# Kernel tuning notes

Measured on AMD Instinct MI355X. Metric: run time of the kernel, lower is better.

Reference implementation:

```python
import jax, jax.numpy as jnp
import numpy as np

ALPHA = 0.2  # LeakyReLU negative slope
OUT_FEATURES = 128


def setup_inputs() -> dict:
    key = jax.random.key(0)
    k1, k2, k3 = jax.random.split(key, 3)
    B, N, F_in, F_out = 4, 4096, 128, OUT_FEATURES
    h = jax.random.normal(k1, (B, N, F_in), dtype=jnp.float32)
    # xavier_uniform with gain 1.414: bound = gain * sqrt(6/(fan_in+fan_out))
    bw = 1.414 * np.sqrt(6.0 / (F_in + F_out))
    W = jax.random.uniform(k2, (F_in, F_out), minval=-bw, maxval=bw, dtype=jnp.float32)
    ba = 1.414 * np.sqrt(6.0 / (2 * F_out + 1))
    a = jax.random.uniform(k3, (2 * F_out, 1), minval=-ba, maxval=ba, dtype=jnp.float32)
    return {"h": h, "W": W, "a": a}


def reference(h, W, a):
    # Wh: [B, N, F_out]
    Wh = jnp.einsum("bni,ij->bnj", h, W)
    a1 = a[:OUT_FEATURES, :]   # [F_out, 1]
    a2 = a[OUT_FEATURES:, :]   # [F_out, 1]
    Wh1 = jnp.einsum("bni,ij->bnj", Wh, a1)  # [B, N, 1]
    Wh2 = jnp.einsum("bni,ij->bnj", Wh, a2)  # [B, N, 1]
    # e: [B, N, N] via broadcast add of column + row vectors
    e = Wh1 + jnp.swapaxes(Wh2, 1, 2)
    e = jax.nn.leaky_relu(e, negative_slope=ALPHA)
    attention = jax.nn.softmax(e, axis=2)
    # dropout is identity in eval mode (p=0.0 / training=False)
    h_prime = jnp.einsum("bij,bjn->bin", attention, Wh)
    return jax.nn.elu(h_prime)
```

## Files before the change

kernel.cpp:

```cpp
#include <hip/hip_runtime.h>
#include <hip/hip_bf16.h>


#define ALPHA 0.2f
#define NN 4096
#define FD 128

typedef __attribute__((ext_vector_type(8))) short s8v;
typedef __attribute__((ext_vector_type(4))) float f4v;
typedef __attribute__((ext_vector_type(2))) unsigned int u2v;
typedef __attribute__((ext_vector_type(4))) unsigned int u4v;

__device__ __forceinline__ unsigned short f2bf(float x) {
  return (unsigned short)((__float_as_uint(x) + 0x8000u) >> 16);
}
__device__ __forceinline__ float bf2f(unsigned short s) {
  return __uint_as_float(((unsigned)s) << 16);
}

__global__ __launch_bounds__(256, 4) void k1_gemm(
    const float* __restrict__ h, const float* __restrict__ W,
    const float* __restrict__ a,
    unsigned short* __restrict__ WhTt,
    float* __restrict__ s1g, float* __restrict__ Eg, float* __restrict__ Fg)
{
  __shared__ __align__(16) unsigned char wls[32768];
  const int tid = threadIdx.x;
  const int b = blockIdx.x >> 6;
  const int j0 = (blockIdx.x & 63) << 6;

#pragma unroll
  for (int it = 0; it < 16; ++it) {
    int cidx = it * 256 + tid;
    int i = cidx >> 5;
    int f0 = (cidx & 31) << 2;
    f4v v = *(const f4v*)(W + (size_t)cidx * 4);
#pragma unroll
    for (int e = 0; e < 4; ++e) {
      int f = f0 + e;
      int byte = f * 256 + (((i >> 3) ^ (f & 15)) << 4) + ((i & 7) << 1);
      *(unsigned short*)(wls + byte) = f2bf(v[e]);
    }
  }
  __syncthreads();

  const int w = tid >> 6, lane = tid & 63;
  const int quad = lane >> 4, lcol = lane & 15;
  const int jrow = j0 + 16 * w + lcol;

  f4v acc[8];
#pragma unroll
  for (int nt = 0; nt < 8; ++nt) acc[nt] = (f4v){0.f, 0.f, 0.f, 0.f};

#pragma unroll
  for (int kk = 0; kk < 4; ++kk) {
    const float* hp = h + (((size_t)(b * NN + jrow)) << 7) + (kk << 5) + (quad << 3);
    f4v v0 = *(const f4v*)hp;
    f4v v1 = *(const f4v*)(hp + 4);
    s8v af;
#pragma unroll
    for (int e = 0; e < 4; ++e) { af[e] = (short)f2bf(v0[e]); af[4+e] = (short)f2bf(v1[e]); }
#pragma unroll
    for (int nt = 0; nt < 8; ++nt) {
      int f = 16 * nt + lcol;
      int slot = ((kk << 2) + quad) ^ (f & 15);
      s8v bfr = *(const s8v*)(wls + (f << 8) + (slot << 4));
      acc[nt] = __builtin_amdgcn_mfma_f32_16x16x32_bf16(af, bfr, acc[nt], 0, 0, 0);
    }
  }

  float s1v[4] = {0,0,0,0}, s2v[4] = {0,0,0,0};
#pragma unroll
  for (int nt = 0; nt < 8; ++nt) {
    float a1 = a[16 * nt + lcol];
    float a2 = a[128 + 16 * nt + lcol];
#pragma unroll
    for (int r = 0; r < 4; ++r) { s1v[r] += acc[nt][r] * a1; s2v[r] += acc[nt][r] * a2; }
  }
#pragma unroll
  for (int r = 0; r < 4; ++r)
#pragma unroll
    for (int d = 1; d < 16; d <<= 1) {
      s1v[r] += __shfl_xor(s1v[r], d, 64);
      s2v[r] += __shfl_xor(s2v[r], d, 64);
    }
  if (lcol == 0) {
    int jb = b * NN + j0 + 16 * w + (quad << 2);
    *(f4v*)(s1g + jb) = (f4v){s1v[0], s1v[1], s1v[2], s1v[3]};
    f4v Ee, Ff;
#pragma unroll
    for (int r = 0; r < 4; ++r) {
      float d = s2v[r] - 8.0f;
      Ee[r] = __expf(d);
      Ff[r] = __expf(ALPHA * d);
    }
    *(f4v*)(Eg + jb) = Ee;
    *(f4v*)(Fg + jb) = Ff;
  }

  {
    const int c = j0 >> 8;
    const int octb = ((j0 & 255) >> 3) + 2 * w + (quad >> 1);
    const int eoff = (quad & 1) << 2;
#pragma unroll
    for (int nt = 0; nt < 8; ++nt) {
      int f = 16 * nt + lcol;
      unsigned u0 = __float_as_uint(acc[nt][0]) + 0x8000u;
      unsigned u1 = __float_as_uint(acc[nt][1]) + 0x8000u;
      unsigned u2 = __float_as_uint(acc[nt][2]) + 0x8000u;
      unsigned u3 = __float_as_uint(acc[nt][3]) + 0x8000u;
      u2v pk;
      pk[0] = (u0 >> 16) | (u1 & 0xFFFF0000u);
      pk[1] = (u2 >> 16) | (u3 & 0xFFFF0000u);
      size_t off = ((((size_t)(b * 16 + c) * 32 + octb) * 128 + f) << 3) + eoff;
      *(u2v*)(WhTt + off) = pk;
    }
  }
}

__global__ __launch_bounds__(256, 2) void k3_split(
    const unsigned short* __restrict__ WhTt,
    const float* __restrict__ s1g,
    const float* __restrict__ Eg,
    const float* __restrict__ Fg,
    unsigned short* __restrict__ pO,
    float* __restrict__ pl)
{
  __shared__ __align__(16) unsigned char smem[24576];
  const int tid = threadIdx.x;
  const int w = tid >> 6, lane = tid & 63;
  const int quad = lane >> 4, lcol = lane & 15;
  const int blk = blockIdx.x;
  const int b = blk >> 7, rg = (blk >> 2) & 31, jq = blk & 3;
  const int irow0 = rg * 128 + w * 32;

  const unsigned short* whtb = WhTt + ((size_t)b << 19);
  const float* Egb = Eg + b * NN + (jq << 10);
  const float* Fgb = Fg + b * NN + (jq << 10);

  float rr[2];
#pragma unroll
  for (int mt = 0; mt < 2; ++mt) {
    float x = s1g[b * NN + irow0 + 16 * mt + lcol] + 8.0f;
    rr[mt] = __expf((ALPHA - 1.0f) * x);
  }

  {
    f4v ve = *(const f4v*)(Egb + tid * 4);
    *(f4v*)(smem + 16384 + tid * 16) = ve;
    f4v vf = *(const f4v*)(Fgb + tid * 4);
    *(f4v*)(smem + 20480 + tid * 16) = vf;
  }

  auto tilePtr = [&](int s) -> const unsigned short* {
    int og0 = (jq << 7) + (s << 2);
    return whtb + (((size_t)(og0 >> 5)) << 15) + ((og0 & 31) << 10);
  };
  {
    const unsigned short* tp = tilePtr(0);
    u4v t0 = *(const u4v*)(tp + tid * 16);
    u4v t1 = *(const u4v*)(tp + tid * 16 + 8);
    *(u4v*)(smem + tid * 32) = t0;
    *(u4v*)(smem + tid * 32 + 16) = t1;
  }

  f4v acc[2][8], accL[2];
#pragma unroll
  for (int mt = 0; mt < 2; ++mt) {
    accL[mt] = (f4v){0.f, 0.f, 0.f, 0.f};
#pragma unroll
    for (int nt = 0; nt < 8; ++nt) acc[mt][nt] = (f4v){0.f, 0.f, 0.f, 0.f};
  }
  s8v ones;
  {
    short o = (lcol == 0) ? (short)0x3F80 : (short)0;
#pragma unroll
    for (int t = 0; t < 8; ++t) ones[t] = o;
  }

  const float* EFb = (const float*)(smem + 16384);

  for (int s = 0; s < 32; ++s) {
    __syncthreads();
    u4v tn0, tn1;
    if (s < 31) {
      const unsigned short* tp = tilePtr(s + 1);
      tn0 = *(const u4v*)(tp + tid * 16);
      tn1 = *(const u4v*)(tp + tid * 16 + 8);
    }
    const unsigned char* buf = smem + ((s & 1) << 13);

    const int jloc = (s << 5) + (quad << 3);
    f4v Ea0 = *(const f4v*)(EFb + jloc);
    f4v Ea1 = *(const f4v*)(EFb + jloc + 4);
    f4v Fa0 = *(const f4v*)(EFb + 1024 + jloc);
    f4v Fa1 = *(const f4v*)(EFb + 1024 + jloc + 4);
    float Ev[8] = {Ea0[0], Ea0[1], Ea0[2], Ea0[3], Ea1[0], Ea1[1], Ea1[2], Ea1[3]};
    float Fv[8] = {Fa0[0], Fa0[1], Fa0[2], Fa0[3], Fa1[0], Fa1[1], Fa1[2], Fa1[3]};

    s8v bfr[8];
#pragma unroll
    for (int nt = 0; nt < 8; ++nt) {
      int f = (nt << 4) + lcol;
      bfr[nt] = *(const s8v*)(buf + (quad << 11) + (f << 4));
    }

    s8v af[2];
#pragma unroll
    for (int mt = 0; mt < 2; ++mt) {
      float R = rr[mt];
      u4v pk4;
#pragma unroll
      for (int t = 0; t < 8; t += 2) {
        float q0 = fmaxf(Ev[t], R * Fv[t]);
        float q1 = fmaxf(Ev[t + 1], R * Fv[t + 1]);
        unsigned u0 = __float_as_uint(q0) + 0x8000u;
        unsigned u1 = __float_as_uint(q1) + 0x8000u;
        pk4[t >> 1] = __builtin_amdgcn_perm(u1, u0, 0x07060302);
      }
      af[mt] = __builtin_bit_cast(s8v, pk4);
    }
#pragma unroll
    for (int nt = 0; nt < 8; ++nt)
#pragma unroll
      for (int mt = 0; mt < 2; ++mt)
        acc[mt][nt] = __builtin_amdgcn_mfma_f32_16x16x32_bf16(af[mt], bfr[nt], acc[mt][nt], 0, 0, 0);
#pragma unroll
    for (int mt = 0; mt < 2; ++mt)
      accL[mt] = __builtin_amdgcn_mfma_f32_16x16x32_bf16(af[mt], ones, accL[mt], 0, 0, 0);

    if (s < 31) {
      unsigned char* dst = smem + (((s + 1) & 1) << 13) + tid * 32;
      *(u4v*)dst = tn0;
      *(u4v*)(dst + 16) = tn1;
    }
  }

  if (lcol == 0) {
#pragma unroll
    for (int mt = 0; mt < 2; ++mt)
#pragma unroll
      for (int r = 0; r < 4; ++r)
        pl[(size_t)blk * 128 + w * 32 + 16 * mt + (quad << 2) + r] = accL[mt][r];
  }
  unsigned short* po = pO + (size_t)blk * 16384;
#pragma unroll
  for (int mt = 0; mt < 2; ++mt)
#pragma unroll
    for (int nt = 0; nt < 8; ++nt) {
      unsigned u0 = __float_as_uint(acc[mt][nt][0]) + 0x8000u;
      unsigned u1 = __float_as_uint(acc[mt][nt][1]) + 0x8000u;
      unsigned u2 = __float_as_uint(acc[mt][nt][2]) + 0x8000u;
      unsigned u3 = __float_as_uint(acc[mt][nt][3]) + 0x8000u;
      u2v pk;
      pk[0] = (u0 >> 16) | (u1 & 0xFFFF0000u);
      pk[1] = (u2 >> 16) | (u3 & 0xFFFF0000u);
      int off = (((w * 2 + mt) * 8) + nt) * 256 + (lane << 2);
      *(u2v*)(po + off) = pk;
    }
}

__global__ __launch_bounds__(256) void k4_comb(
    const unsigned short* __restrict__ pO, const float* __restrict__ pl,
    float* __restrict__ out)
{
  const int tid = threadIdx.x, blk = blockIdx.x;
  const int g = blk >> 1, half = blk & 1;
  const int b = g >> 5, rg = g & 31;
  const int wm = (half << 2) + (tid >> 6);
  const int lane = tid & 63;
  const int quad = lane >> 4, lcol = lane & 15;
  const int kbase = (b << 7) + (rg << 2);

  float il[4];
#pragma unroll
  for (int r = 0; r < 4; ++r) {
    int rowloc = wm * 16 + (quad << 2) + r;
    float l = 0.f;
#pragma unroll
    for (int q = 0; q < 4; ++q) l += pl[(size_t)(kbase + q) * 128 + rowloc];
    il[r] = 1.0f / l;
  }

  const size_t rowg0 = ((size_t)b * NN + rg * 128 + wm * 16 + (quad << 2));
#pragma unroll
  for (int nt = 0; nt < 8; ++nt) {
    const int off = ((wm << 3) + nt) * 256 + (lane << 2);
    float s0 = 0.f, s1 = 0.f, s2 = 0.f, s3 = 0.f;
#pragma unroll
    for (int q = 0; q < 4; ++q) {
      u2v pk = *(const u2v*)(pO + (size_t)(kbase + q) * 16384 + off);
      s0 += __uint_as_float(pk[0] << 16);
      s1 += __uint_as_float(pk[0] & 0xFFFF0000u);
      s2 += __uint_as_float(pk[1] << 16);
      s3 += __uint_as_float(pk[1] & 0xFFFF0000u);
    }
    float v[4] = {s0 * il[0], s1 * il[1], s2 * il[2], s3 * il[3]};
#pragma unroll
    for (int r = 0; r < 4; ++r) {
      float x = v[r];
      x = x > 0.f ? x : (__expf(x) - 1.f);
      out[(rowg0 + r) * 128 + (nt << 4) + lcol] = x;
    }
  }
}

__global__ __launch_bounds__(512, 2) void k3_mono(
    const unsigned short* __restrict__ WhTt,
    const float* __restrict__ s1g,
    const float* __restrict__ Eg,
    const float* __restrict__ Fg,
    float* __restrict__ out)
{
  __shared__ __align__(16) unsigned char smem[33024];
  const int tid = threadIdx.x;
  const int kp = tid >> 6, lane = tid & 63;
  const int quad = lane >> 4, lcol = lane & 15;
  const int b = (blockIdx.x & 7) >> 1;
  const int i0 = ((((blockIdx.x & 1) << 5) | (blockIdx.x >> 3))) << 6;
  const int c0 = (blockIdx.x >> 3) & 15;
  const int oct = (kp << 2) + quad;

  float Ar[4], Br[4];
#pragma unroll
  for (int mt = 0; mt < 4; ++mt) {
    float x = s1g[b * NN + i0 + 16 * mt + lcol] + 8.0f;
    float m = fmaxf(x, ALPHA * x);
    Ar[mt] = __expf(x - m);
    Br[mt] = __expf(ALPHA * x - m);
  }

  f4v acc[4][8], accL[4];
#pragma unroll
  for (int mt = 0; mt < 4; ++mt) {
    accL[mt] = (f4v){0.f, 0.f, 0.f, 0.f};
#pragma unroll
    for (int nt = 0; nt < 8; ++nt) acc[mt][nt] = (f4v){0.f, 0.f, 0.f, 0.f};
  }
  s8v ones;
  {
    short o = (lcol == 0) ? (short)0x3F80 : (short)0;
#pragma unroll
    for (int t = 0; t < 8; ++t) ones[t] = o;
  }

  const unsigned short* whtb = WhTt + ((size_t)b << 19);
  const float* Egb = Eg + b * NN;
  const float* Fgb = Fg + b * NN;
  const int jw = oct << 3;

  f4v Ec0 = *(const f4v*)(Egb + (c0 << 8) + jw);
  f4v Ec1 = *(const f4v*)(Egb + (c0 << 8) + jw + 4);
  f4v Fc0 = *(const f4v*)(Fgb + (c0 << 8) + jw);
  f4v Fc1 = *(const f4v*)(Fgb + (c0 << 8) + jw + 4);

  for (int cc = 0; cc < 16; ++cc) {
    const int c = (cc + c0) & 15;
    const unsigned short* tile = whtb + ((size_t)c << 15) + (oct << 10);
    s8v bfr[8];
#pragma unroll
    for (int nt = 0; nt < 8; ++nt)
      bfr[nt] = *(const s8v*)(tile + (((nt << 4) + lcol) << 3));

    f4v En0, En1, Fn0, Fn1;
    if (cc < 15) {
      int jg = (((cc + 1 + c0) & 15) << 8) + jw;
      En0 = *(const f4v*)(Egb + jg); En1 = *(const f4v*)(Egb + jg + 4);
      Fn0 = *(const f4v*)(Fgb + jg); Fn1 = *(const f4v*)(Fgb + jg + 4);
    }

    float Ev[8] = {Ec0[0], Ec0[1], Ec0[2], Ec0[3], Ec1[0], Ec1[1], Ec1[2], Ec1[3]};
    float Fv[8] = {Fc0[0], Fc0[1], Fc0[2], Fc0[3], Fc1[0], Fc1[1], Fc1[2], Fc1[3]};

    s8v af[4];
#pragma unroll
    for (int mt = 0; mt < 4; ++mt) {
      float A = Ar[mt], Bc = Br[mt];
      u4v pk4;
#pragma unroll
      for (int t = 0; t < 8; t += 2) {
        float p0 = fmaxf(A * Ev[t], Bc * Fv[t]);
        float p1 = fmaxf(A * Ev[t + 1], Bc * Fv[t + 1]);
        unsigned u0 = __float_as_uint(p0) + 0x8000u;
        unsigned u1 = __float_as_uint(p1) + 0x8000u;
        pk4[t >> 1] = __builtin_amdgcn_perm(u1, u0, 0x07060302);
      }
      af[mt] = __builtin_bit_cast(s8v, pk4);
    }
#pragma unroll
    for (int nt = 0; nt < 8; ++nt)
#pragma unroll
      for (int mt = 0; mt < 4; ++mt)
        acc[mt][nt] = __builtin_amdgcn_mfma_f32_16x16x32_bf16(af[mt], bfr[nt], acc[mt][nt], 0, 0, 0);
#pragma unroll
    for (int mt = 0; mt < 4; ++mt)
      accL[mt] = __builtin_amdgcn_mfma_f32_16x16x32_bf16(af[mt], ones, accL[mt], 0, 0, 0);

    Ec0 = En0; Ec1 = En1; Fc0 = Fn0; Fc1 = Fn1;
  }

  float* hsum = (float*)smem;
  float* l_red = (float*)(smem + 32768);
#pragma unroll
  for (int t = 0; t < 4; ++t)
    *(f4v*)(hsum + tid * 16 + t * 4) = (f4v){0.f, 0.f, 0.f, 0.f};
  if (tid < 64) l_red[tid] = 0.f;
  __syncthreads();

#pragma unroll
  for (int mt = 0; mt < 4; ++mt) {
    if (lcol == 0) {
#pragma unroll
      for (int r = 0; r < 4; ++r)
        atomicAdd(&l_red[16 * mt + (quad << 2) + r], accL[mt][r]);
    }
#pragma unroll
    for (int nt = 0; nt < 8; ++nt)
#pragma unroll
      for (int r = 0; r < 4; ++r) {
        int row = 16 * mt + (quad << 2) + r;
        int f = (nt << 4) + lcol;
        int fx = (f + (quad << 3)) & 127;
        atomicAdd(&hsum[(row << 7) + fx], acc[mt][nt][r]);
      }
  }
  __syncthreads();

  {
    int r = tid >> 3;
    int f0 = (tid & 7) << 4;
    int off = ((r >> 2) & 3) << 3;
    float il = 1.0f / l_red[r];
    size_t o = (((size_t)b * NN + i0 + r) << 7) + f0;
#pragma unroll
    for (int t = 0; t < 4; ++t) {
      int fx = (f0 + 4 * t + off) & 127;
      f4v v = *(const f4v*)(hsum + (r << 7) + fx);
      f4v ov;
#pragma unroll
      for (int e = 0; e < 4; ++e) {
        float x = v[e] * il;
        ov[e] = x > 0.f ? x : (__expf(x) - 1.f);
      }
      *(f4v*)(out + o + 4 * t) = ov;
    }
  }
}

extern "C" void kernel_launch(void* const* d_in, const int* in_sizes, int n_in,
                              void* d_out, int out_size, void* d_ws, size_t ws_size,
                              hipStream_t stream) {
  const float* h = (const float*)d_in[0];
  const float* W = (const float*)d_in[1];
  const float* a = (const float*)d_in[2];
  float* out = (float*)d_out;
  unsigned char* ws = (unsigned char*)d_ws;

  unsigned short* WhTt = (unsigned short*)ws;
  float* s1g = (float*)(ws + 4194304);
  float* Eg  = (float*)(ws + 4259840);
  float* Fg  = (float*)(ws + 4325376);
  unsigned short* pO = (unsigned short*)(ws + 4390912);
  float* pl = (float*)(ws + 21168128);
  const size_t NEED_SPLIT = 21430272;
  const size_t NEED_MONO = 4390912;
  if (ws_size < NEED_MONO) return;

  hipLaunchKernelGGL(k1_gemm, dim3(256), dim3(256), 0, stream,
                     h, W, a, WhTt, s1g, Eg, Fg);
  if (ws_size >= NEED_SPLIT) {
    hipLaunchKernelGGL(k3_split, dim3(512), dim3(256), 0, stream,
                       WhTt, s1g, Eg, Fg, pO, pl);
    hipLaunchKernelGGL(k4_comb, dim3(256), dim3(256), 0, stream,
                       pO, pl, out);
  } else {
    hipLaunchKernelGGL(k3_mono, dim3(256), dim3(512), 0, stream,
                       WhTt, s1g, Eg, Fg, out);
  }
}
```

Measured before the change: 106.1 us.

## Fuse GEMM, split attention and combine into one cooperative kernel with grid syncs

Merges the three separate launches (projection GEMM, split-K attention, combine) into a single cooperative kernel of 512 blocks that separates the phases with grid-wide barriers. This is meant to remove the launch gaps and tail effects between the three kernels. In exchange it pays for two grid.sync barriers and a threadfence. The projection phase now runs at the attention kernel's occupancy, and half the blocks sit idle in the first and last phases.

```diff
diff --git a/kernel.cpp b/kernel.cpp
--- a/kernel.cpp
+++ b/kernel.cpp
@@ -1,5 +1,8 @@
 #include <hip/hip_runtime.h>
+#include <hip/hip_cooperative_groups.h>
 #include <hip/hip_bf16.h>
+
+namespace cg = cooperative_groups;
 
 
 #define ALPHA 0.2f
@@ -14,8 +17,292 @@
 __device__ __forceinline__ unsigned short f2bf(float x) {
   return (unsigned short)((__float_as_uint(x) + 0x8000u) >> 16);
 }
-__device__ __forceinline__ float bf2f(unsigned short s) {
-  return __uint_as_float(((unsigned)s) << 16);
+
+__global__ __launch_bounds__(256, 2) void kfused(
+    const float* __restrict__ h, const float* __restrict__ W,
+    const float* __restrict__ a,
+    unsigned short* __restrict__ WhTt,
+    float* __restrict__ s1g, float* __restrict__ Eg, float* __restrict__ Fg,
+    unsigned short* __restrict__ pO,
+    float* __restrict__ pl,
+    float* __restrict__ out)
+{
+  __shared__ __align__(16) unsigned char shm[32768];
+  cg::grid_group grid = cg::this_grid();
+  const int tid = threadIdx.x;
+  const int blk = blockIdx.x;
+  const int lane = tid & 63;
+  const int quad = lane >> 4, lcol = lane & 15;
+
+  if (blk < 256) {
+    unsigned char* wls = shm;
+    const int b = blk >> 6;
+    const int j0 = (blk & 63) << 6;
+
+#pragma unroll
+    for (int it = 0; it < 16; ++it) {
+      int cidx = it * 256 + tid;
+      int i = cidx >> 5;
+      int f0 = (cidx & 31) << 2;
+      f4v v = *(const f4v*)(W + (size_t)cidx * 4);
+#pragma unroll
+      for (int e = 0; e < 4; ++e) {
+        int f = f0 + e;
+        int byte = f * 256 + (((i >> 3) ^ (f & 15)) << 4) + ((i & 7) << 1);
+        *(unsigned short*)(wls + byte) = f2bf(v[e]);
+      }
+    }
+    __syncthreads();
+
+    const int w = tid >> 6;
+    const int jrow = j0 + 16 * w + lcol;
+
+    f4v acc[8];
+#pragma unroll
+    for (int nt = 0; nt < 8; ++nt) acc[nt] = (f4v){0.f, 0.f, 0.f, 0.f};
+
+#pragma unroll
+    for (int kk = 0; kk < 4; ++kk) {
+      const float* hp = h + (((size_t)(b * NN + jrow)) << 7) + (kk << 5) + (quad << 3);
+      f4v v0 = *(const f4v*)hp;
+      f4v v1 = *(const f4v*)(hp + 4);
+      s8v af;
+#pragma unroll
+      for (int e = 0; e < 4; ++e) { af[e] = (short)f2bf(v0[e]); af[4+e] = (short)f2bf(v1[e]); }
+#pragma unroll
+      for (int nt = 0; nt < 8; ++nt) {
+        int f = 16 * nt + lcol;
+        int slot = ((kk << 2) + quad) ^ (f & 15);
+        s8v bfr = *(const s8v*)(wls + (f << 8) + (slot << 4));
+        acc[nt] = __builtin_amdgcn_mfma_f32_16x16x32_bf16(af, bfr, acc[nt], 0, 0, 0);
+      }
+    }
+
+    float s1v[4] = {0,0,0,0}, s2v[4] = {0,0,0,0};
+#pragma unroll
+    for (int nt = 0; nt < 8; ++nt) {
+      float a1 = a[16 * nt + lcol];
+      float a2 = a[128 + 16 * nt + lcol];
+#pragma unroll
+      for (int r = 0; r < 4; ++r) { s1v[r] += acc[nt][r] * a1; s2v[r] += acc[nt][r] * a2; }
+    }
+#pragma unroll
+    for (int r = 0; r < 4; ++r)
+#pragma unroll
+      for (int d = 1; d < 16; d <<= 1) {
+        s1v[r] += __shfl_xor(s1v[r], d, 64);
+        s2v[r] += __shfl_xor(s2v[r], d, 64);
+      }
+    if (lcol == 0) {
+      int jb = b * NN + j0 + 16 * w + (quad << 2);
+      *(f4v*)(s1g + jb) = (f4v){s1v[0], s1v[1], s1v[2], s1v[3]};
+      f4v Ee, Ff;
+#pragma unroll
+      for (int r = 0; r < 4; ++r) {
+        float d = s2v[r] - 8.0f;
+        Ee[r] = __expf(d);
+        Ff[r] = __expf(ALPHA * d);
+      }
+      *(f4v*)(Eg + jb) = Ee;
+      *(f4v*)(Fg + jb) = Ff;
+    }
+
+    {
+      const int c = j0 >> 8;
+      const int octb = ((j0 & 255) >> 3) + 2 * w + (quad >> 1);
+      const int eoff = (quad & 1) << 2;
+#pragma unroll
+      for (int nt = 0; nt < 8; ++nt) {
+        int f = 16 * nt + lcol;
+        unsigned u0 = __float_as_uint(acc[nt][0]) + 0x8000u;
+        unsigned u1 = __float_as_uint(acc[nt][1]) + 0x8000u;
+        unsigned u2 = __float_as_uint(acc[nt][2]) + 0x8000u;
+        unsigned u3 = __float_as_uint(acc[nt][3]) + 0x8000u;
+        u2v pk;
+        pk[0] = (u0 >> 16) | (u1 & 0xFFFF0000u);
+        pk[1] = (u2 >> 16) | (u3 & 0xFFFF0000u);
+        size_t off = ((((size_t)(b * 16 + c) * 32 + octb) * 128 + f) << 3) + eoff;
+        *(u2v*)(WhTt + off) = pk;
+      }
+    }
+  }
+
+  __threadfence();
+  grid.sync();
+
+  {
+    unsigned char* smem = shm;
+    const int w = tid >> 6;
+    const int b = blk >> 7, rg = (blk >> 2) & 31, jq = blk & 3;
+    const int irow0 = rg * 128 + w * 32;
+
+    const unsigned short* whtb = WhTt + ((size_t)b << 19);
+    const float* Egb = Eg + b * NN + (jq << 10);
+    const float* Fgb = Fg + b * NN + (jq << 10);
+
+    float rr[2];
+#pragma unroll
+    for (int mt = 0; mt < 2; ++mt) {
+      float x = s1g[b * NN + irow0 + 16 * mt + lcol] + 8.0f;
+      rr[mt] = __expf((ALPHA - 1.0f) * x);
+    }
+
+    {
+      f4v ve = *(const f4v*)(Egb + tid * 4);
+      *(f4v*)(smem + 16384 + tid * 16) = ve;
+      f4v vf = *(const f4v*)(Fgb + tid * 4);
+      *(f4v*)(smem + 20480 + tid * 16) = vf;
+    }
+
+    auto tilePtr = [&](int s) -> const unsigned short* {
+      int og0 = (jq << 7) + (s << 2);
+      return whtb + (((size_t)(og0 >> 5)) << 15) + ((og0 & 31) << 10);
+    };
+    {
+      const unsigned short* tp = tilePtr(0);
+      u4v t0 = *(const u4v*)(tp + tid * 16);
+      u4v t1 = *(const u4v*)(tp + tid * 16 + 8);
+      *(u4v*)(smem + tid * 32) = t0;
+      *(u4v*)(smem + tid * 32 + 16) = t1;
+    }
+
+    f4v acc[2][8], accL[2];
+#pragma unroll
+    for (int mt = 0; mt < 2; ++mt) {
+      accL[mt] = (f4v){0.f, 0.f, 0.f, 0.f};
+#pragma unroll
+      for (int nt = 0; nt < 8; ++nt) acc[mt][nt] = (f4v){0.f, 0.f, 0.f, 0.f};
+    }
+    s8v ones;
+    {
+      short o = (lcol == 0) ? (short)0x3F80 : (short)0;
+#pragma unroll
+      for (int t = 0; t < 8; ++t) ones[t] = o;
+    }
+
+    const float* EFb = (const float*)(smem + 16384);
+
+    for (int s = 0; s < 32; ++s) {
+      __syncthreads();
+      u4v tn0, tn1;
+      if (s < 31) {
+        const unsigned short* tp = tilePtr(s + 1);
+        tn0 = *(const u4v*)(tp + tid * 16);
+        tn1 = *(const u4v*)(tp + tid * 16 + 8);
+      }
+      const unsigned char* buf = smem + ((s & 1) << 13);
+
+      const int jloc = (s << 5) + (quad << 3);
+      f4v Ea0 = *(const f4v*)(EFb + jloc);
+      f4v Ea1 = *(const f4v*)(EFb + jloc + 4);
+      f4v Fa0 = *(const f4v*)(EFb + 1024 + jloc);
+      f4v Fa1 = *(const f4v*)(EFb + 1024 + jloc + 4);
+      float Ev[8] = {Ea0[0], Ea0[1], Ea0[2], Ea0[3], Ea1[0], Ea1[1], Ea1[2], Ea1[3]};
+      float Fv[8] = {Fa0[0], Fa0[1], Fa0[2], Fa0[3], Fa1[0], Fa1[1], Fa1[2], Fa1[3]};
+
+      s8v bfr[8];
+#pragma unroll
+      for (int nt = 0; nt < 8; ++nt) {
+        int f = (nt << 4) + lcol;
+        bfr[nt] = *(const s8v*)(buf + (quad << 11) + (f << 4));
+      }
+
+      s8v af[2];
+#pragma unroll
+      for (int mt = 0; mt < 2; ++mt) {
+        float R = rr[mt];
+        u4v pk4;
+#pragma unroll
+        for (int t = 0; t < 8; t += 2) {
+          float q0 = fmaxf(Ev[t], R * Fv[t]);
+          float q1 = fmaxf(Ev[t + 1], R * Fv[t + 1]);
+          unsigned u0 = __float_as_uint(q0) + 0x8000u;
+          unsigned u1 = __float_as_uint(q1) + 0x8000u;
+          pk4[t >> 1] = __builtin_amdgcn_perm(u1, u0, 0x07060302);
+        }
+        af[mt] = __builtin_bit_cast(s8v, pk4);
+      }
+#pragma unroll
+      for (int nt = 0; nt < 8; ++nt)
+#pragma unroll
+        for (int mt = 0; mt < 2; ++mt)
+          acc[mt][nt] = __builtin_amdgcn_mfma_f32_16x16x32_bf16(af[mt], bfr[nt], acc[mt][nt], 0, 0, 0);
+#pragma unroll
+      for (int mt = 0; mt < 2; ++mt)
+        accL[mt] = __builtin_amdgcn_mfma_f32_16x16x32_bf16(af[mt], ones, accL[mt], 0, 0, 0);
+
+      if (s < 31) {
+        unsigned char* dst = smem + (((s + 1) & 1) << 13) + tid * 32;
+        *(u4v*)dst = tn0;
+        *(u4v*)(dst + 16) = tn1;
+      }
+    }
+
+    if (lcol == 0) {
+#pragma unroll
+      for (int mt = 0; mt < 2; ++mt)
+#pragma unroll
+        for (int r = 0; r < 4; ++r)
+          pl[(size_t)blk * 128 + w * 32 + 16 * mt + (quad << 2) + r] = accL[mt][r];
+    }
+    unsigned short* po = pO + (size_t)blk * 16384;
+#pragma unroll
+    for (int mt = 0; mt < 2; ++mt)
+#pragma unroll
+      for (int nt = 0; nt < 8; ++nt) {
+        unsigned u0 = __float_as_uint(acc[mt][nt][0]) + 0x8000u;
+        unsigned u1 = __float_as_uint(acc[mt][nt][1]) + 0x8000u;
+        unsigned u2 = __float_as_uint(acc[mt][nt][2]) + 0x8000u;
+        unsigned u3 = __float_as_uint(acc[mt][nt][3]) + 0x8000u;
+        u2v pk;
+        pk[0] = (u0 >> 16) | (u1 & 0xFFFF0000u);
+        pk[1] = (u2 >> 16) | (u3 & 0xFFFF0000u);
+        int off = (((w * 2 + mt) * 8) + nt) * 256 + (lane << 2);
+        *(u2v*)(po + off) = pk;
+      }
+  }
+
+  __threadfence();
+  grid.sync();
+
+  if (blk < 256) {
+    const int g = blk >> 1, half = blk & 1;
+    const int b = g >> 5, rg = g & 31;
+    const int wm = (half << 2) + (tid >> 6);
+    const int kbase = (b << 7) + (rg << 2);
+
+    float il[4];
+#pragma unroll
+    for (int r = 0; r < 4; ++r) {
+      int rowloc = wm * 16 + (quad << 2) + r;
+      float l = 0.f;
+#pragma unroll
+      for (int q = 0; q < 4; ++q) l += pl[(size_t)(kbase + q) * 128 + rowloc];
+      il[r] = 1.0f / l;
+    }
+
+    const size_t rowg0 = ((size_t)b * NN + rg * 128 + wm * 16 + (quad << 2));
+#pragma unroll
+    for (int nt = 0; nt < 8; ++nt) {
+      const int off = ((wm << 3) + nt) * 256 + (lane << 2);
+      float s0 = 0.f, s1 = 0.f, s2 = 0.f, s3 = 0.f;
+#pragma unroll
+      for (int q = 0; q < 4; ++q) {
+        u2v pk = *(const u2v*)(pO + (size_t)(kbase + q) * 16384 + off);
+        s0 += __uint_as_float(pk[0] << 16);
+        s1 += __uint_as_float(pk[0] & 0xFFFF0000u);
+        s2 += __uint_as_float(pk[1] << 16);
+        s3 += __uint_as_float(pk[1] & 0xFFFF0000u);
+      }
+      float v[4] = {s0 * il[0], s1 * il[1], s2 * il[2], s3 * il[3]};
+#pragma unroll
+      for (int r = 0; r < 4; ++r) {
+        float x = v[r];
+        x = x > 0.f ? x : (__expf(x) - 1.f);
+        out[(rowg0 + r) * 128 + (nt << 4) + lcol] = x;
+      }
+    }
+  }
 }
 
 __global__ __launch_bounds__(256, 4) void k1_gemm(
@@ -114,193 +401,6 @@
       pk[1] = (u2 >> 16) | (u3 & 0xFFFF0000u);
       size_t off = ((((size_t)(b * 16 + c) * 32 + octb) * 128 + f) << 3) + eoff;
       *(u2v*)(WhTt + off) = pk;
-    }
-  }
-}
-
-__global__ __launch_bounds__(256, 2) void k3_split(
-    const unsigned short* __restrict__ WhTt,
-    const float* __restrict__ s1g,
-    const float* __restrict__ Eg,
-    const float* __restrict__ Fg,
-    unsigned short* __restrict__ pO,
-    float* __restrict__ pl)
-{
-  __shared__ __align__(16) unsigned char smem[24576];
-  const int tid = threadIdx.x;
-  const int w = tid >> 6, lane = tid & 63;
-  const int quad = lane >> 4, lcol = lane & 15;
-  const int blk = blockIdx.x;
-  const int b = blk >> 7, rg = (blk >> 2) & 31, jq = blk & 3;
-  const int irow0 = rg * 128 + w * 32;
-
-  const unsigned short* whtb = WhTt + ((size_t)b << 19);
-  const float* Egb = Eg + b * NN + (jq << 10);
-  const float* Fgb = Fg + b * NN + (jq << 10);
-
-  float rr[2];
-#pragma unroll
-  for (int mt = 0; mt < 2; ++mt) {
-    float x = s1g[b * NN + irow0 + 16 * mt + lcol] + 8.0f;
-    rr[mt] = __expf((ALPHA - 1.0f) * x);
-  }
-
-  {
-    f4v ve = *(const f4v*)(Egb + tid * 4);
-    *(f4v*)(smem + 16384 + tid * 16) = ve;
-    f4v vf = *(const f4v*)(Fgb + tid * 4);
-    *(f4v*)(smem + 20480 + tid * 16) = vf;
-  }
-
-  auto tilePtr = [&](int s) -> const unsigned short* {
-    int og0 = (jq << 7) + (s << 2);
-    return whtb + (((size_t)(og0 >> 5)) << 15) + ((og0 & 31) << 10);
-  };
-  {
-    const unsigned short* tp = tilePtr(0);
-    u4v t0 = *(const u4v*)(tp + tid * 16);
-    u4v t1 = *(const u4v*)(tp + tid * 16 + 8);
-    *(u4v*)(smem + tid * 32) = t0;
-    *(u4v*)(smem + tid * 32 + 16) = t1;
-  }
-
-  f4v acc[2][8], accL[2];
-#pragma unroll
-  for (int mt = 0; mt < 2; ++mt) {
-    accL[mt] = (f4v){0.f, 0.f, 0.f, 0.f};
-#pragma unroll
-    for (int nt = 0; nt < 8; ++nt) acc[mt][nt] = (f4v){0.f, 0.f, 0.f, 0.f};
-  }
-  s8v ones;
-  {
-    short o = (lcol == 0) ? (short)0x3F80 : (short)0;
-#pragma unroll
-    for (int t = 0; t < 8; ++t) ones[t] = o;
-  }
-
-  const float* EFb = (const float*)(smem + 16384);
-
-  for (int s = 0; s < 32; ++s) {
-    __syncthreads();
-    u4v tn0, tn1;
-    if (s < 31) {
-      const unsigned short* tp = tilePtr(s + 1);
-      tn0 = *(const u4v*)(tp + tid * 16);
-      tn1 = *(const u4v*)(tp + tid * 16 + 8);
-    }
-    const unsigned char* buf = smem + ((s & 1) << 13);
-
-    const int jloc = (s << 5) + (quad << 3);
-    f4v Ea0 = *(const f4v*)(EFb + jloc);
-    f4v Ea1 = *(const f4v*)(EFb + jloc + 4);
-    f4v Fa0 = *(const f4v*)(EFb + 1024 + jloc);
-    f4v Fa1 = *(const f4v*)(EFb + 1024 + jloc + 4);
-    float Ev[8] = {Ea0[0], Ea0[1], Ea0[2], Ea0[3], Ea1[0], Ea1[1], Ea1[2], Ea1[3]};
-    float Fv[8] = {Fa0[0], Fa0[1], Fa0[2], Fa0[3], Fa1[0], Fa1[1], Fa1[2], Fa1[3]};
-
-    s8v bfr[8];
-#pragma unroll
-    for (int nt = 0; nt < 8; ++nt) {
-      int f = (nt << 4) + lcol;
-      bfr[nt] = *(const s8v*)(buf + (quad << 11) + (f << 4));
-    }
-
-    s8v af[2];
-#pragma unroll
-    for (int mt = 0; mt < 2; ++mt) {
-      float R = rr[mt];
-      u4v pk4;
-#pragma unroll
-      for (int t = 0; t < 8; t += 2) {
-        float q0 = fmaxf(Ev[t], R * Fv[t]);
-        float q1 = fmaxf(Ev[t + 1], R * Fv[t + 1]);
-        unsigned u0 = __float_as_uint(q0) + 0x8000u;
-        unsigned u1 = __float_as_uint(q1) + 0x8000u;
-        pk4[t >> 1] = __builtin_amdgcn_perm(u1, u0, 0x07060302);
-      }
-      af[mt] = __builtin_bit_cast(s8v, pk4);
-    }
-#pragma unroll
-    for (int nt = 0; nt < 8; ++nt)
-#pragma unroll
-      for (int mt = 0; mt < 2; ++mt)
-        acc[mt][nt] = __builtin_amdgcn_mfma_f32_16x16x32_bf16(af[mt], bfr[nt], acc[mt][nt], 0, 0, 0);
-#pragma unroll
-    for (int mt = 0; mt < 2; ++mt)
-      accL[mt] = __builtin_amdgcn_mfma_f32_16x16x32_bf16(af[mt], ones, accL[mt], 0, 0, 0);
-
-    if (s < 31) {
-      unsigned char* dst = smem + (((s + 1) & 1) << 13) + tid * 32;
-      *(u4v*)dst = tn0;
-      *(u4v*)(dst + 16) = tn1;
-    }
-  }
-
-  if (lcol == 0) {
-#pragma unroll
-    for (int mt = 0; mt < 2; ++mt)
-#pragma unroll
-      for (int r = 0; r < 4; ++r)
-        pl[(size_t)blk * 128 + w * 32 + 16 * mt + (quad << 2) + r] = accL[mt][r];
-  }
-  unsigned short* po = pO + (size_t)blk * 16384;
-#pragma unroll
-  for (int mt = 0; mt < 2; ++mt)
-#pragma unroll
-    for (int nt = 0; nt < 8; ++nt) {
-      unsigned u0 = __float_as_uint(acc[mt][nt][0]) + 0x8000u;
-      unsigned u1 = __float_as_uint(acc[mt][nt][1]) + 0x8000u;
-      unsigned u2 = __float_as_uint(acc[mt][nt][2]) + 0x8000u;
-      unsigned u3 = __float_as_uint(acc[mt][nt][3]) + 0x8000u;
-      u2v pk;
-      pk[0] = (u0 >> 16) | (u1 & 0xFFFF0000u);
-      pk[1] = (u2 >> 16) | (u3 & 0xFFFF0000u);
-      int off = (((w * 2 + mt) * 8) + nt) * 256 + (lane << 2);
-      *(u2v*)(po + off) = pk;
-    }
-}
-
-__global__ __launch_bounds__(256) void k4_comb(
-    const unsigned short* __restrict__ pO, const float* __restrict__ pl,
-    float* __restrict__ out)
-{
-  const int tid = threadIdx.x, blk = blockIdx.x;
-  const int g = blk >> 1, half = blk & 1;
-  const int b = g >> 5, rg = g & 31;
-  const int wm = (half << 2) + (tid >> 6);
-  const int lane = tid & 63;
-  const int quad = lane >> 4, lcol = lane & 15;
-  const int kbase = (b << 7) + (rg << 2);
-
-  float il[4];
-#pragma unroll
-  for (int r = 0; r < 4; ++r) {
-    int rowloc = wm * 16 + (quad << 2) + r;
-    float l = 0.f;
-#pragma unroll
-    for (int q = 0; q < 4; ++q) l += pl[(size_t)(kbase + q) * 128 + rowloc];
-    il[r] = 1.0f / l;
-  }
-
-  const size_t rowg0 = ((size_t)b * NN + rg * 128 + wm * 16 + (quad << 2));
-#pragma unroll
-  for (int nt = 0; nt < 8; ++nt) {
-    const int off = ((wm << 3) + nt) * 256 + (lane << 2);
-    float s0 = 0.f, s1 = 0.f, s2 = 0.f, s3 = 0.f;
-#pragma unroll
-    for (int q = 0; q < 4; ++q) {
-      u2v pk = *(const u2v*)(pO + (size_t)(kbase + q) * 16384 + off);
-      s0 += __uint_as_float(pk[0] << 16);
-      s1 += __uint_as_float(pk[0] & 0xFFFF0000u);
-      s2 += __uint_as_float(pk[1] << 16);
-      s3 += __uint_as_float(pk[1] & 0xFFFF0000u);
-    }
-    float v[4] = {s0 * il[0], s1 * il[1], s2 * il[2], s3 * il[3]};
-#pragma unroll
-    for (int r = 0; r < 4; ++r) {
-      float x = v[r];
-      x = x > 0.f ? x : (__expf(x) - 1.f);
-      out[(rowg0 + r) * 128 + (nt << 4) + lcol] = x;
     }
   }
 }
@@ -466,14 +566,14 @@
   const size_t NEED_MONO = 4390912;
   if (ws_size < NEED_MONO) return;
 
-  hipLaunchKernelGGL(k1_gemm, dim3(256), dim3(256), 0, stream,
-                     h, W, a, WhTt, s1g, Eg, Fg);
   if (ws_size >= NEED_SPLIT) {
-    hipLaunchKernelGGL(k3_split, dim3(512), dim3(256), 0, stream,
-                       WhTt, s1g, Eg, Fg, pO, pl);
-    hipLaunchKernelGGL(k4_comb, dim3(256), dim3(256), 0, stream,
-                       pO, pl, out);
+    void* args[] = {(void*)&h, (void*)&W, (void*)&a, (void*)&WhTt, (void*)&s1g,
+                    (void*)&Eg, (void*)&Fg, (void*)&pO, (void*)&pl, (void*)&out};
+    hipLaunchCooperativeKernel(reinterpret_cast<const void*>(&kfused),
+                               dim3(512), dim3(256), args, 0, stream);
   } else {
+    hipLaunchKernelGGL(k1_gemm, dim3(256), dim3(256), 0, stream,
+                       h, W, a, WhTt, s1g, Eg, Fg);
     hipLaunchKernelGGL(k3_mono, dim3(256), dim3(512), 0, stream,
                        WhTt, s1g, Eg, Fg, out);
   }
```

New measurement: 327.8 us. 3.09x slower.
